# Performance work log

Measured on AMD Instinct MI355X. Metric: run time of the kernel, lower is better.

## Reference

```python
import jax, jax.numpy as jnp
import numpy as np

SEQ, BATCH = 2048, 32
ENC_HS, DEC_HS = 512, 1024

def setup_inputs() -> dict:
    key = jax.random.key(0)
    k1, k2, k3, k4, k5 = jax.random.split(key, 5)
    return {
        "hidden": jax.random.normal(k1, (BATCH, DEC_HS), dtype=jnp.float32),
        "encoder_outputs": jax.random.normal(k2, (SEQ, BATCH, 2 * ENC_HS), dtype=jnp.float32),
        "attn_w": jax.random.normal(k3, (2 * ENC_HS + DEC_HS, DEC_HS), dtype=jnp.float32) * 0.02,
        "attn_b": jax.random.normal(k4, (DEC_HS,), dtype=jnp.float32) * 0.02,
        "v": jax.random.normal(k5, (DEC_HS,), dtype=jnp.float32),
    }

def reference(hidden, encoder_outputs, attn_w, attn_b, v):
    # encoder_outputs: [S, B, 2*enc_hs] -> [B, S, 2*enc_hs]
    enc = jnp.transpose(encoder_outputs, (1, 0, 2))
    B, S, _ = enc.shape
    # hidden: [B, dec_hs] broadcast to [B, S, dec_hs]
    h = jnp.broadcast_to(hidden[:, None, :], (B, S, hidden.shape[-1]))
    cat = jnp.concatenate([h, enc], axis=2)            # [B, S, 2*enc_hs+dec_hs]
    energy = jnp.tanh(cat @ attn_w + attn_b)            # [B, S, dec_hs]
    scores = jnp.einsum("bsd,d->bs", energy, v)        # [B, S]
    return jax.nn.softmax(scores, axis=1)
```

## Files before the change

kernel.cpp:

```cpp
#include <hip/hip_runtime.h>


typedef _Float16 f16;
typedef _Float16 half8 __attribute__((ext_vector_type(8)));
typedef float f32x4 __attribute__((ext_vector_type(4)));

#define KDIM 1024
#define NDIM 1024
#define SEQ  2048
#define NB   32

typedef __attribute__((address_space(1))) void gvoid;
typedef __attribute__((address_space(3))) void svoid;

__device__ __forceinline__ void gload_lds16(const void* g, void* l) {
    __builtin_amdgcn_global_load_lds((const gvoid*)g, (svoid*)l, 16, 0, 0);
}

__global__ __launch_bounds__(256) void prep_w(const float* __restrict__ w,
                                              f16* __restrict__ wt) {
    int idx   = blockIdx.x * 256 + threadIdx.x;
    int t     = idx >> 11;
    int unit  = idx & 2047;
    int nloc  = unit >> 2;
    int kblk  = unit & 3;
    int kstep = t >> 1, npass = t & 1;
    int n_g   = npass * 512 + nloc;
    int kbase = kstep * 32 + kblk * 8;
    half8 h;
#pragma unroll
    for (int kk = 0; kk < 8; ++kk)
        h[kk] = (f16)w[(size_t)(1024 + kbase + kk) * 1024 + n_g];
    int p = nloc * 4 + ((kblk + (nloc >> 1)) & 3);
    *(half8*)&wt[(size_t)t * 16384 + p * 8] = h;
}

__global__ __launch_bounds__(256) void prep_hb(const float* __restrict__ hidden,
                                               const float* __restrict__ attn_w,
                                               const float* __restrict__ attn_b,
                                               float* __restrict__ hb) {
    int b = blockIdx.x >> 2;
    int n = (blockIdx.x & 3) * 256 + threadIdx.x;
    const float* h = hidden + (size_t)b * 1024;
    float acc = attn_b[n];
#pragma unroll 8
    for (int k = 0; k < 1024; ++k)
        acc += h[k] * attn_w[(size_t)k * 1024 + n];
    hb[(size_t)b * 1024 + n] = acc;
}

__global__ __launch_bounds__(512, 2)
void fused_energy(const float* __restrict__ enc, const f16* __restrict__ wt,
                  const float* __restrict__ hb, const float* __restrict__ vvec,
                  float* __restrict__ out) {
    __shared__ f16 As[128 * 32];
    __shared__ f16 Ws[512 * 32];
    __shared__ float red[4][128];

    const int tid  = threadIdx.x;
    const int lane = tid & 63;
    const int wv   = tid >> 6;
    const int wm   = wv >> 2;
    const int wn   = wv & 3;
    const int l15  = lane & 15;
    const int l4   = lane >> 4;
    const int wgrow = blockIdx.x * 128;

    const int ar  = tid >> 2;
    const int akb = tid & 3;
    const float* aG = enc + (size_t)(wgrow + ar) * KDIM + akb * 8;
    f16* aDst = &As[(ar * 4 + ((akb + (ar >> 1)) & 3)) * 8];

    const int wseg = wv * 4;
    char* wLds = (char*)Ws + wseg * 1024 + lane * 16;

    int aOff[4], bOff[8];
#pragma unroll
    for (int mi = 0; mi < 4; ++mi) {
        int r = wm * 64 + mi * 16 + l15;
        aOff[mi] = (r * 4 + ((l4 + (r >> 1)) & 3)) * 8;
    }
#pragma unroll
    for (int nj = 0; nj < 8; ++nj) {
        int n = wn * 128 + nj * 16 + l15;
        bOff[nj] = (n * 4 + ((l4 + (n >> 1)) & 3)) * 8;
    }

    float part[4][4];
#pragma unroll
    for (int mi = 0; mi < 4; ++mi)
#pragma unroll
        for (int rg = 0; rg < 4; ++rg) part[mi][rg] = 0.f;

    const f32x4 zero = {0.f, 0.f, 0.f, 0.f};

    for (int pass = 0; pass < 2; ++pass) {
        f32x4 acc[4][8];
#pragma unroll
        for (int mi = 0; mi < 4; ++mi)
#pragma unroll
            for (int nj = 0; nj < 8; ++nj) acc[mi][nj] = zero;

        for (int ks = 0; ks < 32; ++ks) {
            f32x4 a0 = *(const f32x4*)(aG + ks * 32);
            f32x4 a1 = *(const f32x4*)(aG + ks * 32 + 4);
            __syncthreads();
            {
                const char* wsrc = (const char*)wt +
                    (size_t)(ks * 2 + pass) * 32768 + wseg * 1024 + lane * 16;
#pragma unroll
                for (int i = 0; i < 4; ++i)
                    gload_lds16(wsrc + i * 1024, wLds + i * 1024);
            }
            half8 ah;
#pragma unroll
            for (int j = 0; j < 4; ++j) ah[j] = (f16)a0[j];
#pragma unroll
            for (int j = 0; j < 4; ++j) ah[4 + j] = (f16)a1[j];
            *(half8*)aDst = ah;
            __syncthreads();

            half8 bf[8];
#pragma unroll
            for (int nj = 0; nj < 8; ++nj) bf[nj] = *(const half8*)&Ws[bOff[nj]];
#pragma unroll
            for (int mi = 0; mi < 4; ++mi) {
                half8 af = *(const half8*)&As[aOff[mi]];
#pragma unroll
                for (int nj = 0; nj < 8; ++nj)
                    acc[mi][nj] = __builtin_amdgcn_mfma_f32_16x16x32_f16(
                        af, bf[nj], acc[mi][nj], 0, 0, 0);
            }
        }

        const int nbase = pass * 512 + wn * 128;
        float vv[8];
#pragma unroll
        for (int nj = 0; nj < 8; ++nj) vv[nj] = vvec[nbase + nj * 16 + l15];
#pragma unroll
        for (int mi = 0; mi < 4; ++mi) {
#pragma unroll
            for (int rg = 0; rg < 4; ++rg) {
                int rl = wm * 64 + mi * 16 + l4 * 4 + rg;
                const float* hbrow = hb + (size_t)(rl & 31) * NDIM + nbase + l15;
                float sum = 0.f;
#pragma unroll
                for (int nj = 0; nj < 8; ++nj) {
                    float e  = acc[mi][nj][rg] + hbrow[nj * 16];
                    float e2 = __expf(2.f * e);
                    float th = 1.f - 2.f / (e2 + 1.f);
                    sum += th * vv[nj];
                }
                part[mi][rg] += sum;
            }
        }
    }

#pragma unroll
    for (int mi = 0; mi < 4; ++mi) {
#pragma unroll
        for (int rg = 0; rg < 4; ++rg) {
            float p = part[mi][rg];
            p += __shfl_xor(p, 1);
            p += __shfl_xor(p, 2);
            p += __shfl_xor(p, 4);
            p += __shfl_xor(p, 8);
            if (l15 == 0) red[wn][wm * 64 + mi * 16 + l4 * 4 + rg] = p;
        }
    }
    __syncthreads();
    if (tid < 128) {
        float s = red[0][tid] + red[1][tid] + red[2][tid] + red[3][tid];
        int rG = wgrow + tid;
        out[(size_t)(rG & 31) * SEQ + (rG >> 5)] = s;
    }
}

__global__ __launch_bounds__(256) void softmax_rows(float* __restrict__ out) {
    const int b = blockIdx.x;
    float* row = out + (size_t)b * SEQ;
    const int tid  = threadIdx.x;
    const int lane = tid & 63;
    const int wv   = tid >> 6;
    __shared__ float sred[4];
    __shared__ float ssum[4];
    float x[8];
    float mx = -3.4e38f;
#pragma unroll
    for (int j = 0; j < 8; ++j) { x[j] = row[tid + j * 256]; mx = fmaxf(mx, x[j]); }
#pragma unroll
    for (int o = 1; o < 64; o <<= 1) mx = fmaxf(mx, __shfl_xor(mx, o));
    if (lane == 0) sred[wv] = mx;
    __syncthreads();
    mx = fmaxf(fmaxf(sred[0], sred[1]), fmaxf(sred[2], sred[3]));
    float s = 0.f;
#pragma unroll
    for (int j = 0; j < 8; ++j) { x[j] = __expf(x[j] - mx); s += x[j]; }
#pragma unroll
    for (int o = 1; o < 64; o <<= 1) s += __shfl_xor(s, o);
    if (lane == 0) ssum[wv] = s;
    __syncthreads();
    s = ssum[0] + ssum[1] + ssum[2] + ssum[3];
    float inv = 1.f / s;
#pragma unroll
    for (int j = 0; j < 8; ++j) row[tid + j * 256] = x[j] * inv;
}

extern "C" void kernel_launch(void* const* d_in, const int* in_sizes, int n_in,
                              void* d_out, int out_size, void* d_ws, size_t ws_size,
                              hipStream_t stream) {
    const float* hidden = (const float*)d_in[0];
    const float* enc    = (const float*)d_in[1];
    const float* attn_w = (const float*)d_in[2];
    const float* attn_b = (const float*)d_in[3];
    const float* v      = (const float*)d_in[4];
    float* out = (float*)d_out;

    f16*   wt = (f16*)d_ws;
    float* hb = (float*)((char*)d_ws + (2u << 20));

    prep_w<<<512, 256, 0, stream>>>(attn_w, wt);
    prep_hb<<<128, 256, 0, stream>>>(hidden, attn_w, attn_b, hb);
    fused_energy<<<512, 512, 0, stream>>>(enc, wt, hb, v, out);
    softmax_rows<<<32, 256, 0, stream>>>(out);
}
```

Before: 284.9 us.

## Retile fused energy GEMM to 256x256 tiles with 4-stage LDS pipeline and N-split partials

Each block now computes a 256-row by 256-column tile, giving 1024 blocks that split N into four quarters and write partial scores to a workspace. Softmax sums the four partials. The K loop is software-pipelined with four LDS buffers for both the W and A tiles, explicit vmcnt/lgkmcnt waits, a single barrier per step and raised wave priority around the MFMAs, so global loads overlap compute. Blocks are also mapped to XCDs for locality. The cost is 128KB of LDS per block, which likely means only one block per CU despite launch bounds of 2, plus extra partial-score traffic.

```diff
diff --git a/kernel.cpp b/kernel.cpp
--- a/kernel.cpp
+++ b/kernel.cpp
@@ -6,9 +6,8 @@
 typedef float f32x4 __attribute__((ext_vector_type(4)));
 
 #define KDIM 1024
-#define NDIM 1024
 #define SEQ  2048
-#define NB   32
+#define MROWS 65536
 
 typedef __attribute__((address_space(1))) void gvoid;
 typedef __attribute__((address_space(3))) void svoid;
@@ -19,20 +18,19 @@
 
 __global__ __launch_bounds__(256) void prep_w(const float* __restrict__ w,
                                               f16* __restrict__ wt) {
-    int idx   = blockIdx.x * 256 + threadIdx.x;
-    int t     = idx >> 11;
-    int unit  = idx & 2047;
-    int nloc  = unit >> 2;
-    int kblk  = unit & 3;
-    int kstep = t >> 1, npass = t & 1;
-    int n_g   = npass * 512 + nloc;
-    int kbase = kstep * 32 + kblk * 8;
+    int idx  = blockIdx.x * 256 + threadIdx.x;
+    int kblk = idx & 3;
+    int nloc = (idx >> 2) & 255;
+    int tile = idx >> 10;
+    int nq   = tile >> 5, ks = tile & 31;
+    int n_g  = nq * 256 + nloc;
+    int kbase = 1024 + ks * 32 + kblk * 8;
     half8 h;
 #pragma unroll
-    for (int kk = 0; kk < 8; ++kk)
-        h[kk] = (f16)w[(size_t)(1024 + kbase + kk) * 1024 + n_g];
+    for (int j = 0; j < 8; ++j)
+        h[j] = (f16)w[(size_t)(kbase + j) * 1024 + n_g];
     int p = nloc * 4 + ((kblk + (nloc >> 1)) & 3);
-    *(half8*)&wt[(size_t)t * 16384 + p * 8] = h;
+    *(half8*)&wt[(size_t)tile * 8192 + p * 8] = h;
 }
 
 __global__ __launch_bounds__(256) void prep_hb(const float* __restrict__ hidden,
@@ -52,10 +50,10 @@
 __global__ __launch_bounds__(512, 2)
 void fused_energy(const float* __restrict__ enc, const f16* __restrict__ wt,
                   const float* __restrict__ hb, const float* __restrict__ vvec,
-                  float* __restrict__ out) {
-    __shared__ f16 As[128 * 32];
-    __shared__ f16 Ws[512 * 32];
-    __shared__ float red[4][128];
+                  float* __restrict__ partout) {
+    __shared__ f16 Ws[4][8192];
+    __shared__ f16 As[4][8192];
+    __shared__ float red[4][256];
 
     const int tid  = threadIdx.x;
     const int lane = tid & 63;
@@ -64,121 +62,160 @@
     const int wn   = wv & 3;
     const int l15  = lane & 15;
     const int l4   = lane >> 4;
-    const int wgrow = blockIdx.x * 128;
-
-    const int ar  = tid >> 2;
-    const int akb = tid & 3;
-    const float* aG = enc + (size_t)(wgrow + ar) * KDIM + akb * 8;
-    f16* aDst = &As[(ar * 4 + ((akb + (ar >> 1)) & 3)) * 8];
-
-    const int wseg = wv * 4;
-    char* wLds = (char*)Ws + wseg * 1024 + lane * 16;
-
-    int aOff[4], bOff[8];
-#pragma unroll
-    for (int mi = 0; mi < 4; ++mi) {
-        int r = wm * 64 + mi * 16 + l15;
-        aOff[mi] = (r * 4 + ((l4 + (r >> 1)) & 3)) * 8;
-    }
-#pragma unroll
-    for (int nj = 0; nj < 8; ++nj) {
-        int n = wn * 128 + nj * 16 + l15;
-        bOff[nj] = (n * 4 + ((l4 + (n >> 1)) & 3)) * 8;
-    }
-
-    float part[4][4];
-#pragma unroll
-    for (int mi = 0; mi < 4; ++mi)
-#pragma unroll
-        for (int rg = 0; rg < 4; ++rg) part[mi][rg] = 0.f;
+
+    const int bid   = blockIdx.x;
+    const int xcd   = bid & 7;
+    const int chunk = bid >> 3;
+    const int mt    = xcd * 32 + (chunk >> 2);
+    const int nq    = chunk & 3;
+    const int mrow0 = mt * 256;
+    const int ncol0 = nq * 256;
+
+    const char* wtNq = (const char*)wt + (size_t)nq * 32 * 16384;
+
+    const int ar  = tid >> 1;
+    const int akp = tid & 1;
+    const float* aG = enc + (size_t)(mrow0 + ar) * KDIM + akp * 16;
+    const int kb0 = akp * 2;
+    const int p0  = ar * 4 + ((kb0 + (ar >> 1)) & 3);
+    const int p1  = ar * 4 + ((kb0 + 1 + (ar >> 1)) & 3);
+
+    const int wOff = wv * 2048 + lane * 16;
+
+    char* const WsB = (char*)&Ws[0][0];
+    char* const AsB = (char*)&As[0][0];
+
+    int aOffB[8], bOffB[4];
+#pragma unroll
+    for (int mi = 0; mi < 8; ++mi) {
+        int r = wm * 128 + mi * 16 + l15;
+        aOffB[mi] = (r * 4 + ((l4 + (r >> 1)) & 3)) * 16;
+    }
+#pragma unroll
+    for (int nj = 0; nj < 4; ++nj) {
+        int n = wn * 64 + nj * 16 + l15;
+        bOffB[nj] = (n * 4 + ((l4 + (n >> 1)) & 3)) * 16;
+    }
 
     const f32x4 zero = {0.f, 0.f, 0.f, 0.f};
-
-    for (int pass = 0; pass < 2; ++pass) {
-        f32x4 acc[4][8];
-#pragma unroll
-        for (int mi = 0; mi < 4; ++mi)
-#pragma unroll
-            for (int nj = 0; nj < 8; ++nj) acc[mi][nj] = zero;
-
-        for (int ks = 0; ks < 32; ++ks) {
-            f32x4 a0 = *(const f32x4*)(aG + ks * 32);
-            f32x4 a1 = *(const f32x4*)(aG + ks * 32 + 4);
-            __syncthreads();
-            {
-                const char* wsrc = (const char*)wt +
-                    (size_t)(ks * 2 + pass) * 32768 + wseg * 1024 + lane * 16;
-#pragma unroll
-                for (int i = 0; i < 4; ++i)
-                    gload_lds16(wsrc + i * 1024, wLds + i * 1024);
+    f32x4 acc[8][4];
+#pragma unroll
+    for (int mi = 0; mi < 8; ++mi)
+#pragma unroll
+        for (int nj = 0; nj < 4; ++nj) acc[mi][nj] = zero;
+
+    f32x4 aE[4], aO[4];
+
+#define STAGE_W(TT)                                                          \
+    {                                                                        \
+        const char* ws_ = wtNq + (size_t)(TT) * 16384 + wOff;                \
+        char* wd_ = WsB + ((TT) & 3) * 16384 + wOff;                         \
+        gload_lds16(ws_, wd_);                                               \
+        gload_lds16(ws_ + 1024, wd_ + 1024);                                 \
+    }
+#define LOAD_A(TT, R)                                                        \
+    {                                                                        \
+        const float* p_ = aG + (TT) * 32;                                    \
+        R[0] = *(const f32x4*)(p_);     R[1] = *(const f32x4*)(p_ + 4);      \
+        R[2] = *(const f32x4*)(p_ + 8); R[3] = *(const f32x4*)(p_ + 12);     \
+    }
+#define WRITE_A(TT, R)                                                       \
+    {                                                                        \
+        half8 h0_, h1_;                                                      \
+        _Pragma("unroll") for (int j = 0; j < 4; ++j) {                      \
+            h0_[j] = (f16)R[0][j]; h0_[4 + j] = (f16)R[1][j];                \
+            h1_[j] = (f16)R[2][j]; h1_[4 + j] = (f16)R[3][j];                \
+        }                                                                    \
+        char* ab_ = AsB + ((TT) & 3) * 16384;                                \
+        *(half8*)(ab_ + p0 * 16) = h0_;                                      \
+        *(half8*)(ab_ + p1 * 16) = h1_;                                      \
+    }
+#define COMPUTE(TT)                                                          \
+    {                                                                        \
+        const char* wb_ = WsB + ((TT) & 3) * 16384;                          \
+        const char* ab_ = AsB + ((TT) & 3) * 16384;                          \
+        half8 bf_[4];                                                        \
+        _Pragma("unroll") for (int nj = 0; nj < 4; ++nj)                     \
+            bf_[nj] = *(const half8*)(wb_ + bOffB[nj]);                      \
+        __builtin_amdgcn_s_setprio(1);                                       \
+        _Pragma("unroll") for (int mi = 0; mi < 8; ++mi) {                   \
+            half8 af_ = *(const half8*)(ab_ + aOffB[mi]);                    \
+            _Pragma("unroll") for (int nj = 0; nj < 4; ++nj)                 \
+                acc[mi][nj] = __builtin_amdgcn_mfma_f32_16x16x32_f16(        \
+                    af_, bf_[nj], acc[mi][nj], 0, 0, 0);                     \
+        }                                                                    \
+        __builtin_amdgcn_s_setprio(0);                                       \
+    }
+
+    STAGE_W(0); LOAD_A(0, aE);
+    STAGE_W(1); LOAD_A(1, aO);
+    asm volatile("s_waitcnt vmcnt(6)" ::: "memory");
+    WRITE_A(0, aE);
+    asm volatile("s_waitcnt lgkmcnt(0)" ::: "memory");
+    __builtin_amdgcn_s_barrier();
+
+    for (int t = 0; t < 30; t += 2) {
+        STAGE_W(t + 2); LOAD_A(t + 2, aE);
+        asm volatile("s_waitcnt vmcnt(6)" ::: "memory");
+        WRITE_A(t + 1, aO);
+        COMPUTE(t);
+        asm volatile("s_waitcnt lgkmcnt(0)" ::: "memory");
+        __builtin_amdgcn_s_barrier();
+
+        STAGE_W(t + 3); LOAD_A(t + 3, aO);
+        asm volatile("s_waitcnt vmcnt(6)" ::: "memory");
+        WRITE_A(t + 2, aE);
+        COMPUTE(t + 1);
+        asm volatile("s_waitcnt lgkmcnt(0)" ::: "memory");
+        __builtin_amdgcn_s_barrier();
+    }
+    asm volatile("s_waitcnt vmcnt(0)" ::: "memory");
+    WRITE_A(31, aO);
+    COMPUTE(30);
+    asm volatile("s_waitcnt lgkmcnt(0)" ::: "memory");
+    __builtin_amdgcn_s_barrier();
+    COMPUTE(31);
+
+#undef STAGE_W
+#undef LOAD_A
+#undef WRITE_A
+#undef COMPUTE
+
+    float vv[4];
+#pragma unroll
+    for (int nj = 0; nj < 4; ++nj) vv[nj] = vvec[ncol0 + wn * 64 + nj * 16 + l15];
+#pragma unroll
+    for (int mi = 0; mi < 8; ++mi) {
+#pragma unroll
+        for (int rg = 0; rg < 4; ++rg) {
+            int rl = wm * 128 + mi * 16 + l4 * 4 + rg;
+            const float* hbrow = hb + (size_t)((mrow0 + rl) & 31) * 1024
+                                 + ncol0 + wn * 64 + l15;
+            float sum = 0.f;
+#pragma unroll
+            for (int nj = 0; nj < 4; ++nj) {
+                float e  = acc[mi][nj][rg] + hbrow[nj * 16];
+                float e2 = __expf(2.f * e);
+                sum += (1.f - 2.f / (e2 + 1.f)) * vv[nj];
             }
-            half8 ah;
-#pragma unroll
-            for (int j = 0; j < 4; ++j) ah[j] = (f16)a0[j];
-#pragma unroll
-            for (int j = 0; j < 4; ++j) ah[4 + j] = (f16)a1[j];
-            *(half8*)aDst = ah;
-            __syncthreads();
-
-            half8 bf[8];
-#pragma unroll
-            for (int nj = 0; nj < 8; ++nj) bf[nj] = *(const half8*)&Ws[bOff[nj]];
-#pragma unroll
-            for (int mi = 0; mi < 4; ++mi) {
-                half8 af = *(const half8*)&As[aOff[mi]];
-#pragma unroll
-                for (int nj = 0; nj < 8; ++nj)
-                    acc[mi][nj] = __builtin_amdgcn_mfma_f32_16x16x32_f16(
-                        af, bf[nj], acc[mi][nj], 0, 0, 0);
-            }
-        }
-
-        const int nbase = pass * 512 + wn * 128;
-        float vv[8];
-#pragma unroll
-        for (int nj = 0; nj < 8; ++nj) vv[nj] = vvec[nbase + nj * 16 + l15];
-#pragma unroll
-        for (int mi = 0; mi < 4; ++mi) {
-#pragma unroll
-            for (int rg = 0; rg < 4; ++rg) {
-                int rl = wm * 64 + mi * 16 + l4 * 4 + rg;
-                const float* hbrow = hb + (size_t)(rl & 31) * NDIM + nbase + l15;
-                float sum = 0.f;
-#pragma unroll
-                for (int nj = 0; nj < 8; ++nj) {
-                    float e  = acc[mi][nj][rg] + hbrow[nj * 16];
-                    float e2 = __expf(2.f * e);
-                    float th = 1.f - 2.f / (e2 + 1.f);
-                    sum += th * vv[nj];
-                }
-                part[mi][rg] += sum;
-            }
-        }
-    }
-
-#pragma unroll
-    for (int mi = 0; mi < 4; ++mi) {
-#pragma unroll
-        for (int rg = 0; rg < 4; ++rg) {
-            float p = part[mi][rg];
+            float p = sum;
             p += __shfl_xor(p, 1);
             p += __shfl_xor(p, 2);
             p += __shfl_xor(p, 4);
             p += __shfl_xor(p, 8);
-            if (l15 == 0) red[wn][wm * 64 + mi * 16 + l4 * 4 + rg] = p;
+            if (l15 == 0) red[wn][rl] = p;
         }
     }
     __syncthreads();
-    if (tid < 128) {
+    if (tid < 256) {
         float s = red[0][tid] + red[1][tid] + red[2][tid] + red[3][tid];
-        int rG = wgrow + tid;
-        out[(size_t)(rG & 31) * SEQ + (rG >> 5)] = s;
-    }
-}
-
-__global__ __launch_bounds__(256) void softmax_rows(float* __restrict__ out) {
+        partout[(size_t)nq * MROWS + mrow0 + tid] = s;
+    }
+}
+
+__global__ __launch_bounds__(256) void softmax_rows(const float* __restrict__ part,
+                                                    float* __restrict__ out) {
     const int b = blockIdx.x;
-    float* row = out + (size_t)b * SEQ;
     const int tid  = threadIdx.x;
     const int lane = tid & 63;
     const int wv   = tid >> 6;
@@ -187,7 +224,13 @@
     float x[8];
     float mx = -3.4e38f;
 #pragma unroll
-    for (int j = 0; j < 8; ++j) { x[j] = row[tid + j * 256]; mx = fmaxf(mx, x[j]); }
+    for (int j = 0; j < 8; ++j) {
+        int flat = (tid + j * 256) * 32 + b;
+        float v = part[flat] + part[MROWS + flat]
+                + part[2 * MROWS + flat] + part[3 * MROWS + flat];
+        x[j] = v;
+        mx = fmaxf(mx, v);
+    }
 #pragma unroll
     for (int o = 1; o < 64; o <<= 1) mx = fmaxf(mx, __shfl_xor(mx, o));
     if (lane == 0) sred[wv] = mx;
@@ -203,7 +246,7 @@
     s = ssum[0] + ssum[1] + ssum[2] + ssum[3];
     float inv = 1.f / s;
 #pragma unroll
-    for (int j = 0; j < 8; ++j) row[tid + j * 256] = x[j] * inv;
+    for (int j = 0; j < 8; ++j) out[(size_t)b * SEQ + tid + j * 256] = x[j] * inv;
 }
 
 extern "C" void kernel_launch(void* const* d_in, const int* in_sizes, int n_in,
@@ -216,11 +259,12 @@
     const float* v      = (const float*)d_in[4];
     float* out = (float*)d_out;
 
-    f16*   wt = (f16*)d_ws;
-    float* hb = (float*)((char*)d_ws + (2u << 20));
+    f16*   wt   = (f16*)d_ws;
+    float* hb   = (float*)((char*)d_ws + 2097152);
+    float* part = (float*)((char*)d_ws + 2097152 + 131072);
 
     prep_w<<<512, 256, 0, stream>>>(attn_w, wt);
     prep_hb<<<128, 256, 0, stream>>>(hidden, attn_w, attn_b, hb);
-    fused_energy<<<512, 512, 0, stream>>>(enc, wt, hb, v, out);
-    softmax_rows<<<32, 256, 0, stream>>>(out);
-}
+    fused_energy<<<1024, 512, 0, stream>>>(enc, wt, hb, v, part);
+    softmax_rows<<<32, 256, 0, stream>>>(part, out);
+}
```

New measurement: 313.3 us. 1.1x slower.
